# Performance work log

Measured on AMD Instinct MI355X. Metric: run time of the kernel, lower is better.

## Reference

```python
import jax, jax.numpy as jnp
import numpy as np

N_KNOTS = 32


def _safe_dist(a, b):
    # a: (B, P, 3), b: (B, M, 3) -> (B, P, M) euclidean distance,
    # with zero (not NaN) gradient at coincident points (diagonal of K_train).
    diff = a[:, :, None, :] - b[:, None, :, :]
    sq = jnp.sum(diff * diff, axis=-1)
    safe = jnp.where(sq > 0, sq, 1.0)
    return jnp.where(sq > 0, jnp.sqrt(safe), 0.0)


def setup_inputs() -> dict:
    key = jax.random.key(0)
    k1, k2 = jax.random.split(key)
    B = 8
    raw = jax.random.uniform(k1, (B, 3, 448, 448), dtype=jnp.float32)
    params_tensor = jax.random.uniform(k2, (B, 6 * N_KNOTS + 3), dtype=jnp.float32)
    return {"raw": raw, "params_tensor": params_tensor}


def reference(raw, params_tensor):
    n = N_KNOTS
    B, C, H, W = raw.shape
    dt = raw.dtype
    # get_params
    xs = params_tensor[:, : 3 * n].reshape(B, n, 3)
    ys = params_tensor[:, 3 * n : 6 * n].reshape(B, n, 3)
    lambdas = params_tensor[:, 6 * n :].reshape(B, 3)
    # NOTE: original code does raw.reshape(B, H*W, C) (NOT a permute) -- replicate exactly.
    fimg = raw.reshape(B, H * W, C)
    # build_k: K_pred (B, HW, n+4)
    d_pred = _safe_dist(fimg, xs)
    K_pred = jnp.concatenate([d_pred, jnp.ones((B, H * W, 1), dt), fimg], axis=2)
    # shared pieces of build_k_train
    dd = _safe_dist(xs, xs)                      # (B, n, n)
    eye = jnp.eye(n, dtype=dt)
    ones_top = jnp.ones((B, n, 1), dt)
    bottom_left = jnp.concatenate([jnp.ones((B, 1, n), dt), jnp.transpose(xs, (0, 2, 1))], axis=1)
    bottom = jnp.concatenate([bottom_left, jnp.zeros((B, 4, 4), dt)], axis=2)  # (B, 4, n+4)
    zs = jnp.zeros((B, 4, 1), dt)
    ws = []
    for i in range(3):  # fixed small channel loop
        d_l = dd + lambdas[:, i][:, None, None] * eye
        top = jnp.concatenate([d_l, ones_top, xs], axis=2)        # (B, n, n+4)
        K = jnp.concatenate([top, bottom], axis=1)                # (B, n+4, n+4)
        v = jnp.concatenate([ys[:, :, i : i + 1], zs], axis=1)    # (B, n+4, 1)
        ws.append(jnp.linalg.pinv(K) @ v)
    Wmat = jnp.concatenate(ws, axis=2)            # (B, n+4, 3)
    out = K_pred @ Wmat                            # (B, HW, 3)
    return out.reshape(raw.shape)
```

## Files before the change

### kernel.cpp

```cpp
#include <hip/hip_runtime.h>
#include <math.h>

#define NK 32
#define NP 36
#define PX 8

__device__ __forceinline__ float hw_sqrtf(float x) {
    return __builtin_amdgcn_sqrtf(x);
}

__device__ __forceinline__ float bcastf(float v, int sl) {
    return __int_as_float(__builtin_amdgcn_readlane(__float_as_int(v), sl));
}

__global__ __launch_bounds__(256, 2) void tps_fused(const float* __restrict__ raw,
                                                    const float* __restrict__ params,
                                                    float* __restrict__ out,
                                                    int HW) {
    __shared__ float  sxs[NK * 3];
    __shared__ float4 sX[NK];
    __shared__ float4 sW4[NP];

    int b   = blockIdx.y;
    int tid = threadIdx.x;
    const float* pp = params + (size_t)b * (6 * NK + 3);

    if (tid < NK * 3) sxs[tid] = pp[tid];
    __syncthreads();

    int wid  = tid >> 6;
    int lane = tid & 63;

    if (wid < 3) {
        int ch = wid;
        float lam = pp[6 * NK + ch];

        int li = (lane < NK) ? lane : 0;
        float myx0 = sxs[li*3+0], myx1 = sxs[li*3+1], myx2 = sxs[li*3+2];

        float rr0,rr1,rr2,rr3,rr4,rr5,rr6,rr7,rr8,rr9,rr10,rr11,rr12,rr13,
              rr14,rr15,rr16,rr17,rr18,rr19,rr20,rr21,rr22,rr23,rr24,rr25,
              rr26,rr27,rr28,rr29,rr30,rr31,rr32,rr33,rr34,rr35,rr36;

        float bcomp = (lane == 33) ? 0.f : (lane == 34) ? 1.f : 2.f;
#define BUILDC(c) do {                                                        \
    float xc0 = sxs[(c)*3+0], xc1 = sxs[(c)*3+1], xc2 = sxs[(c)*3+2];         \
    float dx = myx0 - xc0, dy = myx1 - xc1, dz = myx2 - xc2;                  \
    float d  = hw_sqrtf(dx*dx + dy*dy + dz*dz);                               \
    float v;                                                                  \
    if (lane < NK)       v = (lane == (c)) ? lam : d;                         \
    else if (lane == 32) v = 1.0f;                                            \
    else if (lane < NP)  v = (bcomp==0.f)?xc0:(bcomp==1.f)?xc1:xc2;           \
    else                 v = 0.0f;                                            \
    rr##c = v;                                                                \
} while (0)
        BUILDC(0);  BUILDC(1);  BUILDC(2);  BUILDC(3);  BUILDC(4);  BUILDC(5);
        BUILDC(6);  BUILDC(7);  BUILDC(8);  BUILDC(9);  BUILDC(10); BUILDC(11);
        BUILDC(12); BUILDC(13); BUILDC(14); BUILDC(15); BUILDC(16); BUILDC(17);
        BUILDC(18); BUILDC(19); BUILDC(20); BUILDC(21); BUILDC(22); BUILDC(23);
        BUILDC(24); BUILDC(25); BUILDC(26); BUILDC(27); BUILDC(28); BUILDC(29);
        BUILDC(30); BUILDC(31);
#undef BUILDC
        bool top = (lane < NK);
        rr32 = top ? 1.0f : 0.0f;
        rr33 = top ? myx0 : 0.0f;
        rr34 = top ? myx1 : 0.0f;
        rr35 = top ? myx2 : 0.0f;
        rr36 = top ? pp[3*NK + li*3 + ch] : 0.0f;

#define COLU(c) if ((c) > KK) { rr##c -= minv * bcastf(rr##c, KK); }
#define ALLCOLS \
    COLU(1)  COLU(2)  COLU(3)  COLU(4)  COLU(5)  COLU(6)  COLU(7)  COLU(8)  \
    COLU(9)  COLU(10) COLU(11) COLU(12) COLU(13) COLU(14) COLU(15) COLU(16) \
    COLU(17) COLU(18) COLU(19) COLU(20) COLU(21) COLU(22) COLU(23) COLU(24) \
    COLU(25) COLU(26) COLU(27) COLU(28) COLU(29) COLU(30) COLU(31) COLU(32) \
    COLU(33) COLU(34) COLU(35) COLU(36)
#define STEP(Kv) do {                                                         \
    const int KK = (Kv);                                                      \
    float pv  = bcastf(rr##Kv, (Kv));                                         \
    float inv = __builtin_amdgcn_rcpf(pv);                                    \
    bool  isp = (lane == (Kv));                                               \
    float minv = isp ? (1.0f - inv) : rr##Kv * inv;                           \
    ALLCOLS                                                                   \
} while (0)

        STEP(0);  STEP(1);  STEP(2);  STEP(3);  STEP(4);  STEP(5);
        STEP(6);  STEP(7);  STEP(8);  STEP(9);  STEP(10); STEP(11);
        STEP(12); STEP(13); STEP(14); STEP(15); STEP(16); STEP(17);
        STEP(18); STEP(19); STEP(20); STEP(21); STEP(22); STEP(23);
        STEP(24); STEP(25); STEP(26); STEP(27); STEP(28); STEP(29);
        STEP(30); STEP(31); STEP(32); STEP(33); STEP(34); STEP(35);
#undef STEP
#undef ALLCOLS
#undef COLU

        if (lane < NP)
            ((float*)&sW4[lane])[ch] = rr36;
    } else {
        if (lane < NK)
            sX[lane] = make_float4(sxs[lane*3+0], sxs[lane*3+1], sxs[lane*3+2], 0.f);
    }
    __syncthreads();

    int p8 = blockIdx.x * 256 + tid;
    size_t off = (size_t)b * HW * 3 + (size_t)p8 * (PX * 3);
    const float4* src = (const float4*)(raw + off);
    float f[PX * 3];
    #pragma unroll
    for (int j = 0; j < PX * 3 / 4; ++j) {
        float4 v = src[j];
        f[j*4+0] = v.x; f[j*4+1] = v.y; f[j*4+2] = v.z; f[j*4+3] = v.w;
    }

    float4 wb  = sW4[NK];
    float4 w33 = sW4[NK+1], w34 = sW4[NK+2], w35 = sW4[NK+3];
    float acc[PX * 3];
    #pragma unroll
    for (int p = 0; p < PX; ++p) {
        float c0 = f[p*3+0], c1 = f[p*3+1], c2 = f[p*3+2];
        acc[p*3+0] = wb.x + c0*w33.x + c1*w34.x + c2*w35.x;
        acc[p*3+1] = wb.y + c0*w33.y + c1*w34.y + c2*w35.y;
        acc[p*3+2] = wb.z + c0*w33.z + c1*w34.z + c2*w35.z;
    }

    #pragma unroll 4
    for (int k = 0; k < NK; ++k) {
        float4 x = sX[k];
        float4 w = sW4[k];
        #pragma unroll
        for (int p = 0; p < PX; ++p) {
            float dx = f[p*3+0] - x.x;
            float dy = f[p*3+1] - x.y;
            float dz = f[p*3+2] - x.z;
            float d  = hw_sqrtf(dx*dx + dy*dy + dz*dz);
            acc[p*3+0] += d * w.x;
            acc[p*3+1] += d * w.y;
            acc[p*3+2] += d * w.z;
        }
    }

    float4* dst = (float4*)(out + off);
    #pragma unroll
    for (int j = 0; j < PX * 3 / 4; ++j)
        dst[j] = make_float4(acc[j*4+0], acc[j*4+1], acc[j*4+2], acc[j*4+3]);
}

extern "C" void kernel_launch(void* const* d_in, const int* in_sizes, int n_in,
                              void* d_out, int out_size, void* d_ws, size_t ws_size,
                              hipStream_t stream) {
    const float* raw    = (const float*)d_in[0];
    const float* params = (const float*)d_in[1];
    float* out = (float*)d_out;

    int B  = in_sizes[1] / (6 * NK + 3);
    int HW = in_sizes[0] / (B * 3);

    int groups = HW / PX;
    int bpb = (groups + 255) / 256;
    tps_fused<<<dim3(bpb, B), dim3(256), 0, stream>>>(raw, params, out, HW);
}
```

Baseline: 39.46 us.

## Expand squared distance via norms and pack pairs for dual-issue FMA

Each thread now handles 16 pixels in two chunks of 8, halving the block count so the per-block 36x36 Gauss-Jordan solve is amortised over twice as many pixels. The squared distance is expanded as |f|^2 - 2 f·x + |x|^2, with the -2x and |x|^2 terms precomputed into shared memory. Pixel pairs are kept in float2 form so the compiler can emit packed FMAs. The expansion can lose precision through cancellation, which is why the sum is clamped at zero before the sqrt.

```diff
diff --git a/kernel.cpp b/kernel.cpp
--- a/kernel.cpp
+++ b/kernel.cpp
@@ -3,7 +3,7 @@
 
 #define NK 32
 #define NP 36
-#define PX 8
+#define PX 16
 
 __device__ __forceinline__ float hw_sqrtf(float x) {
     return __builtin_amdgcn_sqrtf(x);
@@ -11,6 +11,13 @@
 
 __device__ __forceinline__ float bcastf(float v, int sl) {
     return __int_as_float(__builtin_amdgcn_readlane(__float_as_int(v), sl));
+}
+
+__device__ __forceinline__ float2 pkf(float s, float2 b, float2 c) {
+    return make_float2(fmaf(s, b.x, c.x), fmaf(s, b.y, c.y));
+}
+__device__ __forceinline__ float2 pkf2(float2 a, float2 b, float2 c) {
+    return make_float2(fmaf(a.x, b.x, c.x), fmaf(a.y, b.y, c.y));
 }
 
 __global__ __launch_bounds__(256, 2) void tps_fused(const float* __restrict__ raw,
@@ -97,52 +104,75 @@
         if (lane < NP)
             ((float*)&sW4[lane])[ch] = rr36;
     } else {
-        if (lane < NK)
-            sX[lane] = make_float4(sxs[lane*3+0], sxs[lane*3+1], sxs[lane*3+2], 0.f);
+        if (lane < NK) {
+            float x0 = sxs[lane*3+0], x1 = sxs[lane*3+1], x2 = sxs[lane*3+2];
+            sX[lane] = make_float4(-2.f*x0, -2.f*x1, -2.f*x2,
+                                   x0*x0 + x1*x1 + x2*x2);
+        }
     }
     __syncthreads();
 
-    int p8 = blockIdx.x * 256 + tid;
-    size_t off = (size_t)b * HW * 3 + (size_t)p8 * (PX * 3);
-    const float4* src = (const float4*)(raw + off);
-    float f[PX * 3];
-    #pragma unroll
-    for (int j = 0; j < PX * 3 / 4; ++j) {
-        float4 v = src[j];
-        f[j*4+0] = v.x; f[j*4+1] = v.y; f[j*4+2] = v.z; f[j*4+3] = v.w;
-    }
+    int p16 = blockIdx.x * 256 + tid;
+    size_t base = (size_t)b * HW * 3 + (size_t)p16 * (PX * 3);
 
     float4 wb  = sW4[NK];
     float4 w33 = sW4[NK+1], w34 = sW4[NK+2], w35 = sW4[NK+3];
-    float acc[PX * 3];
+
     #pragma unroll
-    for (int p = 0; p < PX; ++p) {
-        float c0 = f[p*3+0], c1 = f[p*3+1], c2 = f[p*3+2];
-        acc[p*3+0] = wb.x + c0*w33.x + c1*w34.x + c2*w35.x;
-        acc[p*3+1] = wb.y + c0*w33.y + c1*w34.y + c2*w35.y;
-        acc[p*3+2] = wb.z + c0*w33.z + c1*w34.z + c2*w35.z;
+    for (int j = 0; j < 2; ++j) {
+        const float4* src = (const float4*)(raw + base + j * 24);
+        float4 v0 = src[0], v1 = src[1], v2 = src[2],
+               v3 = src[3], v4 = src[4], v5 = src[5];
+        float f[24] = {v0.x, v0.y, v0.z, v0.w, v1.x, v1.y, v1.z, v1.w,
+                       v2.x, v2.y, v2.z, v2.w, v3.x, v3.y, v3.z, v3.w,
+                       v4.x, v4.y, v4.z, v4.w, v5.x, v5.y, v5.z, v5.w};
+
+        float2 fx[4], fy[4], fz[4], pn[4];
+        #pragma unroll
+        for (int q = 0; q < 4; ++q) {
+            fx[q] = make_float2(f[6*q+0], f[6*q+3]);
+            fy[q] = make_float2(f[6*q+1], f[6*q+4]);
+            fz[q] = make_float2(f[6*q+2], f[6*q+5]);
+            float2 t = make_float2(fx[q].x*fx[q].x, fx[q].y*fx[q].y);
+            t = pkf2(fy[q], fy[q], t);
+            t = pkf2(fz[q], fz[q], t);
+            pn[q] = t;
+        }
+
+        float2 ax[4], ay[4], az[4];
+        #pragma unroll
+        for (int q = 0; q < 4; ++q) {
+            ax[q] = pkf(w35.x, fz[q], pkf(w34.x, fy[q], pkf(w33.x, fx[q], make_float2(wb.x, wb.x))));
+            ay[q] = pkf(w35.y, fz[q], pkf(w34.y, fy[q], pkf(w33.y, fx[q], make_float2(wb.y, wb.y))));
+            az[q] = pkf(w35.z, fz[q], pkf(w34.z, fy[q], pkf(w33.z, fx[q], make_float2(wb.z, wb.z))));
+        }
+
+        #pragma unroll 4
+        for (int k = 0; k < NK; ++k) {
+            float4 xk = sX[k];
+            float4 wk = sW4[k];
+            #pragma unroll
+            for (int q = 0; q < 4; ++q) {
+                float2 t = make_float2(pn[q].x + xk.w, pn[q].y + xk.w);
+                t = pkf(xk.x, fx[q], t);
+                t = pkf(xk.y, fy[q], t);
+                t = pkf(xk.z, fz[q], t);
+                float2 d = make_float2(hw_sqrtf(fmaxf(t.x, 0.f)),
+                                       hw_sqrtf(fmaxf(t.y, 0.f)));
+                ax[q] = pkf(wk.x, d, ax[q]);
+                ay[q] = pkf(wk.y, d, ay[q]);
+                az[q] = pkf(wk.z, d, az[q]);
+            }
+        }
+
+        float4* dst = (float4*)(out + base + j * 24);
+        dst[0] = make_float4(ax[0].x, ay[0].x, az[0].x, ax[0].y);
+        dst[1] = make_float4(ay[0].y, az[0].y, ax[1].x, ay[1].x);
+        dst[2] = make_float4(az[1].x, ax[1].y, ay[1].y, az[1].y);
+        dst[3] = make_float4(ax[2].x, ay[2].x, az[2].x, ax[2].y);
+        dst[4] = make_float4(ay[2].y, az[2].y, ax[3].x, ay[3].x);
+        dst[5] = make_float4(az[3].x, ax[3].y, ay[3].y, az[3].y);
     }
-
-    #pragma unroll 4
-    for (int k = 0; k < NK; ++k) {
-        float4 x = sX[k];
-        float4 w = sW4[k];
-        #pragma unroll
-        for (int p = 0; p < PX; ++p) {
-            float dx = f[p*3+0] - x.x;
-            float dy = f[p*3+1] - x.y;
-            float dz = f[p*3+2] - x.z;
-            float d  = hw_sqrtf(dx*dx + dy*dy + dz*dz);
-            acc[p*3+0] += d * w.x;
-            acc[p*3+1] += d * w.y;
-            acc[p*3+2] += d * w.z;
-        }
-    }
-
-    float4* dst = (float4*)(out + off);
-    #pragma unroll
-    for (int j = 0; j < PX * 3 / 4; ++j)
-        dst[j] = make_float4(acc[j*4+0], acc[j*4+1], acc[j*4+2], acc[j*4+3]);
 }
 
 extern "C" void kernel_launch(void* const* d_in, const int* in_sizes, int n_in,
```

Measured after the change: 36.17 us. 1.09x faster.
